# Optimization experiments

Measured on AMD Instinct MI355X. Metric: run time of the kernel, lower is better.

## Reference

```python
import jax, jax.numpy as jnp
import numpy as np
from jax.scipy.special import logsumexp

B, T, V, D, HD, L = 64, 512, 100000, 300, 256, 9
H = HD // 2  # per-direction hidden size


def _lstm_dir(x, w_ih, w_hh, b_ih, b_hh, reverse):
    # x: [T, B, in]; PyTorch LSTM gate order: i, f, g, o
    xp = jnp.einsum('tbd,gd->tbg', x, w_ih) + b_ih + b_hh  # [T,B,4H]

    def step(carry, xt):
        h, c = carry
        g = xt + h @ w_hh.T
        i, f, gg, o = jnp.split(g, 4, axis=-1)
        c = jax.nn.sigmoid(f) * c + jax.nn.sigmoid(i) * jnp.tanh(gg)
        h = jax.nn.sigmoid(o) * jnp.tanh(c)
        return (h, c), h

    Bn = x.shape[1]
    init = (jnp.zeros((Bn, H), x.dtype), jnp.zeros((Bn, H), x.dtype))
    _, hs = jax.lax.scan(step, init, xp, reverse=reverse)
    return hs  # [T,B,H]


def _bilstm_layer(x, w_ih, w_hh, b_ih, b_hh):
    hf = _lstm_dir(x, w_ih[0], w_hh[0], b_ih[0], b_hh[0], False)
    hb = _lstm_dir(x, w_ih[1], w_hh[1], b_ih[1], b_hh[1], True)
    return jnp.concatenate([hf, hb], axis=-1)  # [T,B,2H]


def _crf_nll(em, tags, mask, start_t, end_t, trans):
    # em: [B,T,L] emissions; torchcrf log-likelihood with reduction='sum'
    mf = mask.astype(em.dtype)
    em_sel = jnp.take_along_axis(em, tags[:, :, None], axis=2)[..., 0]  # [B,T]
    num = start_t[tags[:, 0]] + em_sel[:, 0]
    tr = trans[tags[:, :-1], tags[:, 1:]]  # [B,T-1]
    num = num + ((tr + em_sel[:, 1:]) * mf[:, 1:]).sum(axis=1)
    seq_ends = mask.sum(axis=1) - 1
    last_tags = jnp.take_along_axis(tags, seq_ends[:, None], axis=1)[:, 0]
    num = num + end_t[last_tags]

    # log-partition via scan over time
    alpha0 = start_t[None, :] + em[:, 0]  # [B,L]

    def step(alpha, inp):
        em_t, m_t = inp  # [B,L], [B]
        nxt = logsumexp(alpha[:, :, None] + trans[None] + em_t[:, None, :], axis=1)
        return jnp.where(m_t[:, None], nxt, alpha), None

    alpha, _ = jax.lax.scan(step, alpha0,
                            (em[:, 1:].transpose(1, 0, 2), mask[:, 1:].T))
    denom = logsumexp(alpha + end_t[None, :], axis=1)
    llh = (num - denom).sum()
    return -llh  # model returns -loss (NLL)


def setup_inputs() -> dict:
    key = jax.random.key(0)
    ks = jax.random.split(key, 18)
    w = lambda k, s: jax.random.normal(k, s, dtype=jnp.float32) * 0.08
    inp = {
        'word_batch': jax.random.randint(ks[0], (B, T), 1, V),  # >=1 so mask is all-true
        'label_batch': jax.random.randint(ks[1], (B, T), 0, L),
        'emb': jax.random.normal(ks[2], (V, D), dtype=jnp.float32) * 0.1,
        'w_ih_l0': w(ks[3], (2, 4 * H, D)),
        'w_hh_l0': w(ks[4], (2, 4 * H, H)),
        'b_ih_l0': w(ks[5], (2, 4 * H)),
        'b_hh_l0': w(ks[6], (2, 4 * H)),
        'w_ih_l1': w(ks[7], (2, 4 * H, HD)),
        'w_hh_l1': w(ks[8], (2, 4 * H, H)),
        'b_ih_l1': w(ks[9], (2, 4 * H)),
        'b_hh_l1': w(ks[10], (2, 4 * H)),
        'w_out': w(ks[11], (L, HD)),
        'b_out': w(ks[12], (L,)),
        'start_t': w(ks[13], (L,)),
        'end_t': w(ks[14], (L,)),
        'trans': w(ks[15], (L, L)),
    }
    return inp


def reference(word_batch, label_batch, emb,
              w_ih_l0, w_hh_l0, b_ih_l0, b_hh_l0,
              w_ih_l1, w_hh_l1, b_ih_l1, b_hh_l1,
              w_out, b_out, start_t, end_t, trans):
    mask = word_batch > 0  # [B,T], all-true by construction
    x = emb[word_batch].transpose(1, 0, 2)  # [T,B,D] (dropout is eval no-op)
    x = _bilstm_layer(x, w_ih_l0, w_hh_l0, b_ih_l0, b_hh_l0)
    x = _bilstm_layer(x, w_ih_l1, w_hh_l1, b_ih_l1, b_hh_l1)
    em = jnp.einsum('tbh,lh->btl', x, w_out) + b_out  # [B,T,L]
    return _crf_nll(em, label_batch, mask, start_t, end_t, trans)
```

## Files before the change

### kernel.cpp

```cpp
#include <hip/hip_runtime.h>

#define TT 512
#define NB 64
#define HH 128
#define G4 512
#define HDIM 256

typedef __bf16 bf16x8 __attribute__((ext_vector_type(8)));
typedef float f32x4 __attribute__((ext_vector_type(4)));
typedef unsigned int u32x4 __attribute__((ext_vector_type(4)));
typedef unsigned int u32x2 __attribute__((ext_vector_type(2)));

union FragU { u32x4 u4; bf16x8 bf; unsigned short us[8]; };
union XPU { u32x2 v; unsigned short us[4]; };

#define SC_SIG  -1.442695041f
#define SC_TANH -2.885390082f

__device__ __forceinline__ unsigned short f2bf(float f){
  unsigned u = __builtin_bit_cast(unsigned, f);
  return (unsigned short)((u + 0x7FFFu + ((u>>16)&1u)) >> 16);
}
__device__ __forceinline__ float bf2f(unsigned short h){
  unsigned u = ((unsigned)h) << 16;
  return __builtin_bit_cast(float, u);
}
__device__ __forceinline__ float rsig(float y){
  return __builtin_amdgcn_rcpf(1.0f + __builtin_amdgcn_exp2f(y));
}


__global__ __launch_bounds__(256) void k_prep(
    const float* __restrict__ bi0, const float* __restrict__ bh0,
    const float* __restrict__ bi1, const float* __restrict__ bh1,
    const float* __restrict__ w_ih0, const float* __restrict__ w_ih1,
    float* __restrict__ bias0, float* __restrict__ bias1,
    unsigned short* __restrict__ Bp0, unsigned short* __restrict__ Bp1)
{
  int id = blockIdx.x*256 + threadIdx.x;
  if (id < 2048){
    int n = id & 511;
    float s = ((n >> 7) == 2) ? SC_TANH : SC_SIG;
    if (id < 1024) bias0[id] = (bi0[id] + bh0[id]) * s;
    else { int k = id - 1024; bias1[k] = (bi1[k] + bh1[k]) * s; }
    return;
  }
  id -= 2048;
  if (id < 320*1024){
    int k = id >> 10, c = id & 1023;
    int dir = c >> 9, n = c & 511;
    float s = ((n >> 7) == 2) ? SC_TANH : SC_SIG;
    float v = (k < 300) ? w_ih0[((size_t)(dir*512 + n))*300 + k] * s : 0.f;
    Bp0[(((size_t)(k>>3))*1024 + c)*8 + (k&7)] = f2bf(v);
    return;
  }
  id -= 320*1024;
  if (id < 256*1024){
    int k = id >> 10, c = id & 1023;
    int dir = c >> 9, n = c & 511;
    float s = ((n >> 7) == 2) ? SC_TANH : SC_SIG;
    float v = w_ih1[((size_t)(dir*512 + n))*256 + k] * s;
    Bp1[(((size_t)(k>>3))*1024 + c)*8 + (k&7)] = f2bf(v);
  }
}

__global__ __launch_bounds__(320) void k_embed(
    const int* __restrict__ word, const float* __restrict__ emb,
    unsigned short* __restrict__ xe)
{
  int row = blockIdx.x;
  int c = threadIdx.x;
  int t = row >> 6, b = row & 63;
  int wd = word[b*TT + t];
  float v = (c < 300) ? emb[(size_t)wd*300 + c] : 0.f;
  xe[(size_t)row*320 + c] = f2bf(v);
}


__global__ __launch_bounds__(256) void k_gemm(
    const unsigned short* __restrict__ A,
    const unsigned short* __restrict__ Bp,
    const float* __restrict__ bias,
    unsigned short* __restrict__ xp,
    const int lda, const int KB)
{
  const int tid = threadIdx.x;
  const int l = tid & 63, w = tid >> 6;
  const int quad = l >> 4, lo = l & 15;
  const int wm = w >> 1, wn = w & 1;
  const int M0 = blockIdx.x * 128;
  const int N0 = blockIdx.y * 128;

  __shared__ __align__(16) unsigned short Asl[4*128*8];
  __shared__ __align__(16) unsigned short Bsl[4*128*8];

  f32x4 acc[4][4] = {};

  for (int kb=0; kb<KB; ++kb){
    const int k0 = kb*32;
    u32x4 va[2], vb[2];
    #pragma unroll
    for (int hh=0; hh<2; ++hh){
      const int cch = tid + hh*256;
      const int q = cch >> 7, mm = cch & 127;
      va[hh] = *(const u32x4*)(A + (size_t)(M0+mm)*lda + k0 + q*8);
      vb[hh] = *(const u32x4*)(Bp + (((size_t)((k0>>3)+q))*1024 + N0 + mm)*8);
    }
    __syncthreads();
    #pragma unroll
    for (int hh=0; hh<2; ++hh){
      const int cch = tid + hh*256;
      *(u32x4*)&Asl[cch*8] = va[hh];
      *(u32x4*)&Bsl[cch*8] = vb[hh];
    }
    __syncthreads();

    FragU af[4], bfg[4];
    #pragma unroll
    for (int mt=0; mt<4; ++mt)
      af[mt].u4 = *(const u32x4*)&Asl[((quad<<7) + wm*64 + mt*16 + lo)*8];
    #pragma unroll
    for (int nt=0; nt<4; ++nt)
      bfg[nt].u4 = *(const u32x4*)&Bsl[((quad<<7) + wn*64 + nt*16 + lo)*8];
    #pragma unroll
    for (int mt=0; mt<4; ++mt)
      #pragma unroll
      for (int nt=0; nt<4; ++nt)
        acc[mt][nt] = __builtin_amdgcn_mfma_f32_16x16x32_bf16(af[mt].bf, bfg[nt].bf, acc[mt][nt], 0, 0, 0);
  }

  #pragma unroll
  for (int mt=0; mt<4; ++mt){
    #pragma unroll
    for (int nt=0; nt<4; ++nt){
      const int col = N0 + wn*64 + nt*16 + lo;
      const int dir = col >> 9, n = col & 511;
      const int g = n >> 7, u = n & 127;
      const float bv = bias[col];
      #pragma unroll
      for (int r=0; r<4; ++r){
        const int row = M0 + wm*64 + mt*16 + quad*4 + r;
        const size_t o = (size_t)row*1024 + dir*512 + u*4 + g;
        xp[o] = f2bf(acc[mt][nt][r] + bv);
      }
    }
  }
}


__global__ __launch_bounds__(256, 1) void k_scan(
    const float* __restrict__ w_hh,
    const unsigned short* __restrict__ xp,
    unsigned short* __restrict__ xout)
{
  const int bid = blockIdx.x;
  const int dir = bid >> 5, bg = bid & 31;
  const int tid = threadIdx.x;
  const int l = tid & 63, w = tid >> 6;
  const int quad = l >> 4, lo = l & 15;
  const int qb = quad & 1;
  const int qh = quad >> 1;
  const int uu = w*32 + qh*16 + lo;
  const int bglob = bg*2 + qb;

  FragU bw[8][4];
  {
    const float* wb = w_hh + (size_t)dir*G4*HH;
    #pragma unroll
    for (int nt=0; nt<8; ++nt){
      const int g = nt >> 1;
      const float s = (g == 2) ? SC_TANH : SC_SIG;
      const int grow = g*HH + w*32 + (nt&1)*16 + lo;
      #pragma unroll
      for (int kq=0; kq<4; ++kq){
        const float* p = wb + (size_t)grow*HH + kq*32 + quad*8;
        #pragma unroll
        for (int j=0; j<8; ++j) bw[nt][kq].us[j] = f2bf(p[j] * s);
      }
    }
  }

  __shared__ __align__(16) unsigned short hbuf[2][2][160];
  for (int i = tid; i < 2*2*160; i += 256) ((unsigned short*)hbuf)[i] = 0;
  __syncthreads();

  float c = 0.f;
  const int t0 = dir ? (TT-1) : 0;
  const int dt = dir ? -1 : 1;
  const unsigned short* xpb = xp + (size_t)bglob*1024 + dir*512 + uu*4;
  unsigned short* xob = xout + (size_t)bglob*HDIM + dir*HH + uu;

  u32x2 pf[4];
  #pragma unroll
  for (int k=0; k<4; ++k)
    pf[k] = *(const u32x2*)(xpb + (size_t)(t0 + dt*k)*65536);

  const f32x4 zero4 = {0.f, 0.f, 0.f, 0.f};

  for (int ob=0; ob<TT/4; ++ob){
    #pragma unroll
    for (int ph=0; ph<4; ++ph){
      const int it = ob*4 + ph;
      const int t = t0 + dt*it;
      const int rb = ph & 1;
      const int wb2 = rb ^ 1;

      FragU af[4];
      #pragma unroll
      for (int kq=0; kq<4; ++kq)
        af[kq].u4 = *(const u32x4*)&hbuf[rb][lo & 1][kq*32 + quad*8];

      f32x4 acc[8];
      #pragma unroll
      for (int nt=0; nt<8; ++nt)
        acc[nt] = __builtin_amdgcn_mfma_f32_16x16x32_bf16(af[0].bf, bw[nt][0].bf, zero4, 0, 0, 0);
      #pragma unroll
      for (int kq=1; kq<4; ++kq)
        #pragma unroll
        for (int nt=0; nt<8; ++nt)
          acc[nt] = __builtin_amdgcn_mfma_f32_16x16x32_bf16(af[kq].bf, bw[nt][kq].bf, acc[nt], 0, 0, 0);

      XPU xu; xu.v = pf[ph];
      {
        const int itp = (it+4 < TT) ? (it+4) : (TT-1);
        pf[ph] = *(const u32x2*)(xpb + (size_t)(t0 + dt*itp)*65536);
      }

      float gv[4];
      #pragma unroll
      for (int g=0; g<4; ++g){
        float ta = qb ? acc[g*2  ][1] : acc[g*2  ][0];
        float tb = qb ? acc[g*2+1][1] : acc[g*2+1][0];
        gv[g] = (qh ? tb : ta) + bf2f(xu.us[g]);
      }

      float si = rsig(gv[0]), sf = rsig(gv[1]);
      float tg = __builtin_fmaf(2.0f, rsig(gv[2]), -1.0f);
      float so = rsig(gv[3]);
      c = __builtin_fmaf(sf, c, si*tg);
      float h = so * __builtin_fmaf(2.0f, rsig(SC_TANH*c), -1.0f);
      unsigned short hb = f2bf(h);
      hbuf[wb2][qb][uu] = hb;
      xob[(size_t)t*NB*HDIM] = hb;

      asm volatile("s_waitcnt lgkmcnt(0)\n\ts_barrier" ::: "memory");
    }
  }
}


__global__ __launch_bounds__(256) void k_em(
    const unsigned short* __restrict__ x2,
    const float* __restrict__ w_out,
    const float* __restrict__ b_out,
    float* __restrict__ em)
{
  const int tid = threadIdx.x;
  const int l = tid & 63, w = tid >> 6;
  const int quad = l >> 4, lo = l & 15;
  const int M0 = blockIdx.x*128 + w*32;

  FragU bf[8];
  #pragma unroll
  for (int kq=0; kq<8; ++kq){
    #pragma unroll
    for (int j=0; j<8; ++j){
      float v = (lo < 9) ? w_out[lo*HDIM + kq*32 + quad*8 + j] : 0.f;
      bf[kq].us[j] = f2bf(v);
    }
  }

  f32x4 acc[2] = {};
  #pragma unroll
  for (int kq=0; kq<8; ++kq){
    FragU a0, a1;
    a0.u4 = *(const u32x4*)(x2 + ((size_t)(M0 + lo))*HDIM + kq*32 + quad*8);
    a1.u4 = *(const u32x4*)(x2 + ((size_t)(M0 + 16 + lo))*HDIM + kq*32 + quad*8);
    acc[0] = __builtin_amdgcn_mfma_f32_16x16x32_bf16(a0.bf, bf[kq].bf, acc[0], 0, 0, 0);
    acc[1] = __builtin_amdgcn_mfma_f32_16x16x32_bf16(a1.bf, bf[kq].bf, acc[1], 0, 0, 0);
  }

  if (lo < 9){
    const float bo = b_out[lo];
    #pragma unroll
    for (int mt=0; mt<2; ++mt){
      #pragma unroll
      for (int r=0; r<4; ++r){
        const int row = M0 + mt*16 + quad*4 + r;
        const int t = row >> 6, b = row & 63;
        em[((size_t)b*TT + t)*9 + lo] = acc[mt][r] + bo;
      }
    }
  }
}


__global__ __launch_bounds__(128) void k_crf_r1f(
    const int* __restrict__ word, const float* __restrict__ em,
    const float* __restrict__ start_t, const float* __restrict__ trans,
    float* __restrict__ dst)
{
  const int bid = blockIdx.x;
  const int b = bid >> 6, g = bid & 63;
  const int tid = threadIdx.x;
  const int t0 = g*8;
  __shared__ float R[2][81];
  __shared__ float emsh[8][9];
  __shared__ int wsh[8];
  if (tid < 72){
    int s = tid/9, j = tid - (tid/9)*9;
    emsh[s][j] = em[((size_t)b*TT + t0+s)*9 + j];
  }
  if (tid < 8) wsh[tid] = word[b*TT + t0 + tid];
  __syncthreads();
  int i=0, j=0; float tr[9];
  if (tid < 81){
    i = tid/9; j = tid - i*9;
    #pragma unroll
    for (int k=0;k<9;++k) tr[k] = trans[k*9+j];
    float v;
    if (t0 == 0) v = start_t[j] + emsh[0][j];
    else if (wsh[0] > 0) v = tr[i] + emsh[0][j];
    else v = (i==j) ? 0.f : -1e30f;
    R[0][tid] = v;
  }
  int cur = 0;
  for (int s=1; s<8; ++s){
    __syncthreads();
    if (tid < 81){
      if (wsh[s] > 0){
        float a[9], mx = -3.0e38f;
        #pragma unroll
        for (int k=0;k<9;++k){ a[k] = R[cur][i*9+k] + tr[k]; mx = fmaxf(mx, a[k]); }
        float sm = 0.f;
        #pragma unroll
        for (int k=0;k<9;++k) sm += __expf(a[k]-mx);
        R[cur^1][tid] = mx + __logf(sm) + emsh[s][j];
      } else {
        R[cur^1][tid] = R[cur][tid];
      }
    }
    cur ^= 1;
  }
  __syncthreads();
  if (tid < 81) dst[((size_t)bid)*81 + tid] = R[cur][tid];
}

__global__ __launch_bounds__(128) void k_crf_reduce(
    const float* __restrict__ src, float* __restrict__ dst, const int nm)
{
  const int bid = blockIdx.x;
  const int ng = nm >> 3;
  const int b = bid / ng, g = bid - b*ng;
  const int tid = threadIdx.x;
  __shared__ float R[2][81];
  const float* base = src + ((size_t)b*nm + g*8)*81;
  if (tid < 81) R[0][tid] = base[tid];
  int cur = 0;
  for (int s=1; s<8; ++s){
    __syncthreads();
    if (tid < 81){
      int i = tid/9, j = tid - (tid/9)*9;
      const float* M = base + (size_t)s*81;
      float a[9], mx = -3.0e38f;
      #pragma unroll
      for (int k=0;k<9;++k){ a[k] = R[cur][i*9+k] + M[k*9+j]; mx = fmaxf(mx, a[k]); }
      float sm = 0.f;
      #pragma unroll
      for (int k=0;k<9;++k) sm += __expf(a[k]-mx);
      R[cur^1][tid] = mx + __logf(sm);
    }
    cur ^= 1;
  }
  __syncthreads();
  if (tid < 81) dst[((size_t)b*ng + g)*81 + tid] = R[cur][tid];
}

__global__ __launch_bounds__(256) void k_crf_num(
    const int* __restrict__ word, const int* __restrict__ label,
    const float* __restrict__ em, const float* __restrict__ start_t,
    const float* __restrict__ end_t, const float* __restrict__ trans,
    float* __restrict__ numv)
{
  const int b = blockIdx.x, tid = threadIdx.x;
  __shared__ float sred[256];
  __shared__ int ssend;
  int ms = 0;
  for (int t=tid; t<TT; t+=256) ms += (word[b*TT+t] > 0) ? 1 : 0;
  sred[tid] = (float)ms;
  __syncthreads();
  for (int st=128; st>0; st>>=1){ if (tid<st) sred[tid] += sred[tid+st]; __syncthreads(); }
  if (tid==0) ssend = (int)sred[0] - 1;
  __syncthreads();
  const int send = ssend;
  float part = 0.f;
  for (int t=tid; t<TT; t+=256){
    int tag = label[b*TT+t];
    float es = em[((size_t)b*TT+t)*9 + tag];
    if (t == 0) part += start_t[tag] + es;
    else if (word[b*TT+t] > 0) part += trans[label[b*TT+t-1]*9 + tag] + es;
    if (t == send) part += end_t[tag];
  }
  __syncthreads();
  sred[tid] = part;
  __syncthreads();
  for (int st=128; st>0; st>>=1){ if (tid<st) sred[tid] += sred[tid+st]; __syncthreads(); }
  if (tid==0) numv[b] = sred[0];
}

__global__ __launch_bounds__(64) void k_final(
    const float* __restrict__ numv, const float* __restrict__ G3,
    const float* __restrict__ end_t, float* __restrict__ out)
{
  const int b = threadIdx.x;
  float a[9], mx = -3.0e38f;
  #pragma unroll
  for (int j=0;j<9;++j){ a[j] = G3[b*81 + j] + end_t[j]; mx = fmaxf(mx, a[j]); }
  float sm = 0.f;
  #pragma unroll
  for (int j=0;j<9;++j) sm += __expf(a[j]-mx);
  float denom = mx + __logf(sm);
  float v = numv[b] - denom;
  #pragma unroll
  for (int off=32; off>0; off>>=1) v += __shfl_down(v, off, 64);
  if (b == 0) out[0] = -v;
}


extern "C" void kernel_launch(void* const* d_in, const int* in_sizes, int n_in,
                              void* d_out, int out_size, void* d_ws, size_t ws_size,
                              hipStream_t stream)
{
  (void)in_sizes; (void)n_in; (void)out_size; (void)ws_size;
  const int*   word  = (const int*)d_in[0];
  const int*   label = (const int*)d_in[1];
  const float* emb   = (const float*)d_in[2];
  const float* w_ih0 = (const float*)d_in[3];
  const float* w_hh0 = (const float*)d_in[4];
  const float* b_ih0 = (const float*)d_in[5];
  const float* b_hh0 = (const float*)d_in[6];
  const float* w_ih1 = (const float*)d_in[7];
  const float* w_hh1 = (const float*)d_in[8];
  const float* b_ih1 = (const float*)d_in[9];
  const float* b_hh1 = (const float*)d_in[10];
  const float* w_out = (const float*)d_in[11];
  const float* b_out = (const float*)d_in[12];
  const float* start_t = (const float*)d_in[13];
  const float* end_t   = (const float*)d_in[14];
  const float* trans   = (const float*)d_in[15];

  char* ws = (char*)d_ws;
  unsigned short* xp    = (unsigned short*)(ws + 0);
  unsigned short* xe    = (unsigned short*)(ws + 67108864);
  unsigned short* x1    = (unsigned short*)(ws + 88080384);
  unsigned short* x2    = (unsigned short*)(ws + 104857600);
  unsigned short* Bp0   = (unsigned short*)(ws + 121634816);
  unsigned short* Bp1   = (unsigned short*)(ws + 122290176);
  float*          bias0 = (float*)(ws + 122814464);
  float*          bias1 = (float*)(ws + 122818560);
  float*          em    = (float*)(ws + 122822656);
  float*          G1    = (float*)(ws + 124002304);
  float*          G2    = (float*)(ws + 125329408);
  float*          G3    = (float*)(ws + 125495296);
  float*          numv  = (float*)(ws + 125516032);

  hipLaunchKernelGGL(k_prep, dim3(2312), dim3(256), 0, stream,
                     b_ih0, b_hh0, b_ih1, b_hh1, w_ih0, w_ih1, bias0, bias1, Bp0, Bp1);
  hipLaunchKernelGGL(k_embed, dim3(32768), dim3(320), 0, stream, word, emb, xe);
  hipLaunchKernelGGL(k_gemm, dim3(256, 8), dim3(256), 0, stream, xe, Bp0, bias0, xp, 320, 10);
  hipLaunchKernelGGL(k_scan, dim3(64), dim3(256), 0, stream, w_hh0, xp, x1);
  hipLaunchKernelGGL(k_gemm, dim3(256, 8), dim3(256), 0, stream, x1, Bp1, bias1, xp, 256, 8);
  hipLaunchKernelGGL(k_scan, dim3(64), dim3(256), 0, stream, w_hh1, xp, x2);
  hipLaunchKernelGGL(k_em, dim3(256), dim3(256), 0, stream, x2, w_out, b_out, em);
  hipLaunchKernelGGL(k_crf_r1f, dim3(4096), dim3(128), 0, stream, word, em, start_t, trans, G1);
  hipLaunchKernelGGL(k_crf_reduce, dim3(512), dim3(128), 0, stream, G1, G2, 64);
  hipLaunchKernelGGL(k_crf_reduce, dim3(64), dim3(128), 0, stream, G2, G3, 8);
  hipLaunchKernelGGL(k_crf_num, dim3(64), dim3(256), 0, stream, word, label, em, start_t, end_t, trans, numv);
  hipLaunchKernelGGL(k_final, dim3(1), dim3(64), 0, stream, numv, G3, end_t, (float*)d_out);
}
```

Before: 874.5 us.

## Interleave final MFMA k-step with gate activations in LSTM scan and remap lanes

Splits the last K-chunk of the recurrent MFMA so that each gate's activation (i, g, then f, then o) is computed as soon as its accumulators finish, overlapping transcendental work with the remaining MFMAs on the serial critical path. It also swaps the quad-to-batch/unit mapping so each lane reads element 0 of its accumulator and the hbuf row is indexed by lo>>3. The software bf16 rounding is replaced with the hardware v_cvt_pk_bf16_f32 instruction. The gate inputs are unpacked to float before the MFMAs are issued. The lane remap has to stay consistent with the MFMA output layout; an error there would silently corrupt results.

```diff
diff --git a/kernel.cpp b/kernel.cpp
--- a/kernel.cpp
+++ b/kernel.cpp
@@ -27,6 +27,11 @@
 }
 __device__ __forceinline__ float rsig(float y){
   return __builtin_amdgcn_rcpf(1.0f + __builtin_amdgcn_exp2f(y));
+}
+__device__ __forceinline__ unsigned short f2bf_hw(float f){
+  unsigned p;
+  asm("v_cvt_pk_bf16_f32 %0, %1, %2" : "=v"(p) : "v"(f), "v"(f));
+  return (unsigned short)p;
 }
 
 
@@ -158,8 +163,8 @@
   const int tid = threadIdx.x;
   const int l = tid & 63, w = tid >> 6;
   const int quad = l >> 4, lo = l & 15;
-  const int qb = quad & 1;
-  const int qh = quad >> 1;
+  const int qb = quad >> 1;
+  const int qh = quad & 1;
   const int uu = w*32 + qh*16 + lo;
   const int bglob = bg*2 + qb;
 
@@ -208,38 +213,45 @@
       FragU af[4];
       #pragma unroll
       for (int kq=0; kq<4; ++kq)
-        af[kq].u4 = *(const u32x4*)&hbuf[rb][lo & 1][kq*32 + quad*8];
-
-      f32x4 acc[8];
-      #pragma unroll
-      for (int nt=0; nt<8; ++nt)
-        acc[nt] = __builtin_amdgcn_mfma_f32_16x16x32_bf16(af[0].bf, bw[nt][0].bf, zero4, 0, 0, 0);
-      #pragma unroll
-      for (int kq=1; kq<4; ++kq)
-        #pragma unroll
-        for (int nt=0; nt<8; ++nt)
-          acc[nt] = __builtin_amdgcn_mfma_f32_16x16x32_bf16(af[kq].bf, bw[nt][kq].bf, acc[nt], 0, 0, 0);
+        af[kq].u4 = *(const u32x4*)&hbuf[rb][lo >> 3][kq*32 + quad*8];
 
       XPU xu; xu.v = pf[ph];
+      const float xuf0 = bf2f(xu.us[0]);
+      const float xuf1 = bf2f(xu.us[1]);
+      const float xuf2 = bf2f(xu.us[2]);
+      const float xuf3 = bf2f(xu.us[3]);
       {
         const int itp = (it+4 < TT) ? (it+4) : (TT-1);
         pf[ph] = *(const u32x2*)(xpb + (size_t)(t0 + dt*itp)*65536);
       }
 
-      float gv[4];
-      #pragma unroll
-      for (int g=0; g<4; ++g){
-        float ta = qb ? acc[g*2  ][1] : acc[g*2  ][0];
-        float tb = qb ? acc[g*2+1][1] : acc[g*2+1][0];
-        gv[g] = (qh ? tb : ta) + bf2f(xu.us[g]);
-      }
-
-      float si = rsig(gv[0]), sf = rsig(gv[1]);
-      float tg = __builtin_fmaf(2.0f, rsig(gv[2]), -1.0f);
-      float so = rsig(gv[3]);
+      f32x4 acc[8];
+      #pragma unroll
+      for (int nt=0; nt<8; ++nt)
+        acc[nt] = __builtin_amdgcn_mfma_f32_16x16x32_bf16(af[0].bf, bw[nt][0].bf, zero4, 0, 0, 0);
+      #pragma unroll
+      for (int kq=1; kq<3; ++kq)
+        #pragma unroll
+        for (int nt=0; nt<8; ++nt)
+          acc[nt] = __builtin_amdgcn_mfma_f32_16x16x32_bf16(af[kq].bf, bw[nt][kq].bf, acc[nt], 0, 0, 0);
+
+      acc[0] = __builtin_amdgcn_mfma_f32_16x16x32_bf16(af[3].bf, bw[0][3].bf, acc[0], 0, 0, 0);
+      acc[1] = __builtin_amdgcn_mfma_f32_16x16x32_bf16(af[3].bf, bw[1][3].bf, acc[1], 0, 0, 0);
+      acc[4] = __builtin_amdgcn_mfma_f32_16x16x32_bf16(af[3].bf, bw[4][3].bf, acc[4], 0, 0, 0);
+      acc[5] = __builtin_amdgcn_mfma_f32_16x16x32_bf16(af[3].bf, bw[5][3].bf, acc[5], 0, 0, 0);
+      const float si = rsig((qh ? acc[1][0] : acc[0][0]) + xuf0);
+      const float tg = __builtin_fmaf(2.0f, rsig((qh ? acc[5][0] : acc[4][0]) + xuf2), -1.0f);
+      acc[2] = __builtin_amdgcn_mfma_f32_16x16x32_bf16(af[3].bf, bw[2][3].bf, acc[2], 0, 0, 0);
+      acc[3] = __builtin_amdgcn_mfma_f32_16x16x32_bf16(af[3].bf, bw[3][3].bf, acc[3], 0, 0, 0);
+      const float sf = rsig((qh ? acc[3][0] : acc[2][0]) + xuf1);
       c = __builtin_fmaf(sf, c, si*tg);
-      float h = so * __builtin_fmaf(2.0f, rsig(SC_TANH*c), -1.0f);
-      unsigned short hb = f2bf(h);
+      const float tb = __builtin_fmaf(2.0f, rsig(SC_TANH*c), -1.0f);
+      acc[6] = __builtin_amdgcn_mfma_f32_16x16x32_bf16(af[3].bf, bw[6][3].bf, acc[6], 0, 0, 0);
+      acc[7] = __builtin_amdgcn_mfma_f32_16x16x32_bf16(af[3].bf, bw[7][3].bf, acc[7], 0, 0, 0);
+      const float so = rsig((qh ? acc[7][0] : acc[6][0]) + xuf3);
+
+      const float h = so * tb;
+      const unsigned short hb = f2bf_hw(h);
       hbuf[wb2][qb][uu] = hb;
       xob[(size_t)t*NB*HDIM] = hb;
 
```

New measurement: 823.9 us. 5.8% less time.
